# Optimization experiments

Hardware: AMD Instinct MI355X
Metric: run time of the kernel (lower is better)

## Reference

```python
import jax, jax.numpy as jnp
import numpy as np

NUM_CODES = 4096
TEMPERATURE = 1.0
EPS = 1e-08


def setup_inputs() -> dict:
    key = jax.random.key(0)
    k1, k2, k3 = jax.random.split(key, 3)
    B, D, T = 16, 512, 1500
    encoder_stride = 320
    student_features = jax.random.normal(k1, (B, D, T), dtype=jnp.float32)
    codebook = jax.random.normal(k2, (NUM_CODES, D), dtype=jnp.float32)
    lengths = jax.random.randint(k3, (B,), 0, T * encoder_stride, dtype=jnp.int64)
    return {
        "student_features": student_features,
        "codebook": codebook,
        "lengths": lengths,
        "encoder_stride": encoder_stride,
    }


def _length_mask(lengths, T, stride):
    # frame t is valid iff t < floor(length / stride)  -> (B, T) float mask
    n_valid = jnp.minimum(lengths // stride, T)
    return (jnp.arange(T)[None, :] < n_valid[:, None]).astype(jnp.float32)


def reference(student_features, codebook, lengths, encoder_stride):
    B, D, T = student_features.shape
    mask = _length_mask(lengths, T, encoder_stride)            # (B, T)
    z = jnp.transpose(student_features, (0, 2, 1)).reshape(-1, D)  # (N, D), N = B*T
    # Euclidean cdist via ||z||^2 + ||c||^2 - 2 z c^T (same as torch.cdist GEMM path)
    z2 = jnp.sum(z * z, axis=-1, keepdims=True)                # (N, 1)
    c2 = jnp.sum(codebook * codebook, axis=-1)                 # (K,)
    d2 = z2 + c2[None, :] - 2.0 * (z @ codebook.T)             # (N, K)
    distances = jnp.sqrt(jnp.maximum(d2, 1e-12))
    logits = -distances / TEMPERATURE
    probs = jax.nn.softmax(logits, axis=-1)                    # (N, K)
    probs_masked = probs * mask.reshape(-1, 1)
    code_dist = jnp.sum(probs_masked, axis=0)                  # (K,)
    code_dist = code_dist / (jnp.sum(code_dist) + EPS)
    entropy = -jnp.sum(code_dist * jnp.log(code_dist + EPS))
    max_entropy = jnp.log(jnp.float32(NUM_CODES))
    return 1.0 - entropy / max_entropy
```

## Files before the change

kernel.cpp:

```cpp
#include <hip/hip_runtime.h>
#include <hip/hip_bf16.h>

#define NUM_B   16
#define DIM     512
#define TT      1500
#define NROWS   (NUM_B * TT)
#define NCODES  4096
#define ROW_TILES ((NROWS + 127) / 128)
#define NROWS_PAD (ROW_TILES * 128)
#define NSLICE  8
#define SHIFTC  30.0f

typedef __bf16 bf16x8 __attribute__((ext_vector_type(8)));
typedef float  floatx4 __attribute__((ext_vector_type(4)));
typedef unsigned short ushortx8 __attribute__((ext_vector_type(8)));

__device__ __forceinline__ void glds16(const void* g, void* l) {
    __builtin_amdgcn_global_load_lds(
        (__attribute__((address_space(1))) void*)(void*)g,
        (__attribute__((address_space(3))) void*)l, 16, 0, 0);
}

__global__ void k_transpose(const float* __restrict__ sf, unsigned short* __restrict__ zbf,
                            float* __restrict__ z2) {
    __shared__ float tile[32][33];
    int tid = threadIdx.x;
    int b = blockIdx.z, d0 = blockIdx.y * 32, t0 = blockIdx.x * 32;
    int tl = tid & 31, dg = tid >> 5;
#pragma unroll
    for (int p = 0; p < 4; ++p) {
        int dl = p * 8 + dg;
        int t = t0 + tl;
        if (t < TT) tile[tl][dl] = sf[(size_t)(b * DIM + d0 + dl) * TT + t];
    }
    __syncthreads();
    int dl = tid & 31, tg = tid >> 5;
#pragma unroll
    for (int p = 0; p < 4; ++p) {
        int tl2 = p * 8 + tg;
        int t = t0 + tl2;
        float ssq = 0.f;
        if (t < TT) {
            __hip_bfloat16 h = __float2bfloat16(tile[tl2][dl]);
            zbf[(size_t)(b * TT + t) * DIM + d0 + dl] = __builtin_bit_cast(unsigned short, h);
            float vb = __bfloat162float(h);
            ssq = vb * vb;
        }
        ssq += __shfl_xor(ssq, 16); ssq += __shfl_xor(ssq, 8);
        ssq += __shfl_xor(ssq, 4);  ssq += __shfl_xor(ssq, 2);
        ssq += __shfl_xor(ssq, 1);
        if (dl == 0 && t < TT) atomicAdd(&z2[b * TT + t], ssq);
    }
}

__global__ void k_cb(const float* __restrict__ cb, unsigned short* __restrict__ cbbf,
                     float* __restrict__ c2) {
    int k = blockIdx.x * 4 + (threadIdx.x >> 6);
    int lane = threadIdx.x & 63;
    const float4* src = (const float4*)(cb + (size_t)k * DIM + lane * 8);
    float4 a = src[0], b2 = src[1];
    float vals[8] = {a.x, a.y, a.z, a.w, b2.x, b2.y, b2.z, b2.w};
    float s = 0.f;
    unsigned int h[8];
#pragma unroll
    for (int i = 0; i < 8; ++i) {
        __hip_bfloat16 hb = __float2bfloat16(vals[i]);
        h[i] = __builtin_bit_cast(unsigned short, hb);
        float vb = __bfloat162float(hb);
        s += vb * vb;
    }
    uint4 o;
    o.x = h[0] | (h[1] << 16); o.y = h[2] | (h[3] << 16);
    o.z = h[4] | (h[5] << 16); o.w = h[6] | (h[7] << 16);
    *(uint4*)(cbbf + (size_t)k * DIM + lane * 8) = o;
#pragma unroll
    for (int off = 32; off >= 1; off >>= 1) s += __shfl_down(s, off);
    if (lane == 0) c2[k] = s;
}

__global__ __launch_bounds__(256, 2) void k_gemm1(
    const unsigned short* __restrict__ zbf, const unsigned short* __restrict__ cbbf,
    const float* __restrict__ z2, const float* __restrict__ c2,
    const int* __restrict__ lengths, const int* __restrict__ stride_p,
    float* __restrict__ Sg, unsigned short* __restrict__ Eg) {
    __shared__ unsigned short As[128 * 64];
    __shared__ unsigned short Bs[128 * 64];
    __shared__ float z2s[128], c2s[128];
    __shared__ unsigned char vldp[128];
    __shared__ int s_any;
    int tid = threadIdx.x;
    int r0 = blockIdx.y * 128, c0 = blockIdx.x * 128;
    if (tid == 0) s_any = 0;
    __syncthreads();
    if (tid < 128) {
        int n = r0 + tid;
        int valid = 0;
        if (n < NROWS) {
            int b = n / TT, t = n - b * TT;
            int stride = stride_p[0];
            int nv = lengths[b] / stride;
            if (nv > TT) nv = TT;
            valid = (t < nv);
        }
        if (valid) atomicOr(&s_any, 1);
        vldp[tid] = (unsigned char)valid;
        z2s[tid] = z2[r0 + tid];
        c2s[tid] = c2[c0 + tid];
    }
    __syncthreads();
    if (!s_any) return;

    int wave = tid >> 6, lane = tid & 63;
    int l15 = lane & 15, l4 = lane >> 4;
    int wr = (wave >> 1) * 64, wc = (wave & 1) * 64;

    int srow = lane >> 3;
    int scg = (lane & 7) ^ srow;
    const unsigned short* ag = zbf + (size_t)(r0 + wave * 32 + srow) * DIM + scg * 8;
    const unsigned short* bg = cbbf + (size_t)(c0 + wave * 32 + srow) * DIM + scg * 8;
    unsigned short* al = As + (wave * 32) * 64;
    unsigned short* bl = Bs + (wave * 32) * 64;

    floatx4 acc[4][4];
    const floatx4 zero = {0.f, 0.f, 0.f, 0.f};
#pragma unroll
    for (int i = 0; i < 4; ++i)
#pragma unroll
        for (int j = 0; j < 4; ++j) acc[i][j] = zero;

    int sw = l15 & 7;

    for (int kc = 0; kc < 8; ++kc) {
#pragma unroll
        for (int q = 0; q < 4; ++q) {
            glds16(ag + (size_t)q * 8 * DIM + kc * 64, al + q * 8 * 64);
            glds16(bg + (size_t)q * 8 * DIM + kc * 64, bl + q * 8 * 64);
        }
        __syncthreads();
#pragma unroll
        for (int ks = 0; ks < 64; ks += 32) {
            int g = (ks >> 3) + l4;
            int pcg = g ^ sw;
            bf16x8 av[4], bv[4];
#pragma unroll
            for (int i = 0; i < 4; ++i)
                av[i] = __builtin_bit_cast(bf16x8,
                    *(const ushortx8*)&As[(wr + 16 * i + l15) * 64 + pcg * 8]);
#pragma unroll
            for (int j = 0; j < 4; ++j)
                bv[j] = __builtin_bit_cast(bf16x8,
                    *(const ushortx8*)&Bs[(wc + 16 * j + l15) * 64 + pcg * 8]);
#pragma unroll
            for (int i = 0; i < 4; ++i)
#pragma unroll
                for (int j = 0; j < 4; ++j)
                    acc[i][j] = __builtin_amdgcn_mfma_f32_16x16x32_bf16(av[i], bv[j], acc[i][j], 0, 0, 0);
        }
        __syncthreads();
    }

#pragma unroll
    for (int i = 0; i < 4; ++i) {
#pragma unroll
        for (int r = 0; r < 4; ++r) {
            int rl = wr + 16 * i + 4 * l4 + r;
            bool rv = vldp[rl] != 0;
            float z2v = z2s[rl];
            float s = 0.f;
            unsigned int hh[4];
#pragma unroll
            for (int j = 0; j < 4; ++j) {
                int cl = wc + 16 * j + l15;
                float d2 = fmaf(-2.0f, acc[i][j][r], z2v + c2s[cl]);
                float d = sqrtf(fmaxf(d2, 1e-12f));
                float e = __expf(SHIFTC - d);
                s += e;
                hh[j] = __builtin_bit_cast(unsigned short, __float2bfloat16(e));
            }
            if (rv) {
                uint2 pk;
                pk.x = hh[0] | (hh[1] << 16);
                pk.y = hh[2] | (hh[3] << 16);
                *(uint2*)(Eg + (size_t)(r0 + rl) * NCODES + c0 + wc + l15 * 4) = pk;
            }
            s += __shfl_xor(s, 1); s += __shfl_xor(s, 2);
            s += __shfl_xor(s, 4); s += __shfl_xor(s, 8);
            if (l15 == 0 && rv) atomicAdd(&Sg[r0 + rl], s);
        }
    }
}

__global__ __launch_bounds__(256) void k_scan(
    const unsigned short* __restrict__ Eg, const float* __restrict__ Sg,
    const int* __restrict__ lengths, const int* __restrict__ stride_p,
    float* __restrict__ cdp) {
    __shared__ float rs[32];
    __shared__ int s_any;
    int tid = threadIdx.x;
    int r0 = blockIdx.y * 32;
    if (tid == 0) s_any = 0;
    __syncthreads();
    if (tid < 32) {
        int n = r0 + tid;
        int valid = 0;
        if (n < NROWS) {
            int b = n / TT, t = n - b * TT;
            int nv = lengths[b] / stride_p[0];
            if (nv > TT) nv = TT;
            valid = (t < nv);
        }
        if (valid) atomicOr(&s_any, 1);
        rs[tid] = valid ? 1.0f / Sg[n] : 0.0f;
    }
    __syncthreads();
    if (!s_any) return;

    int p0 = blockIdx.x * 2048 + tid * 8;
    float acc[8] = {0.f, 0.f, 0.f, 0.f, 0.f, 0.f, 0.f, 0.f};
    for (int nn = 0; nn < 32; ++nn) {
        float rn = rs[nn];
        if (rn == 0.f) continue;
        uint4 v = *(const uint4*)(Eg + (size_t)(r0 + nn) * NCODES + p0);
        unsigned int u[4] = {v.x, v.y, v.z, v.w};
#pragma unroll
        for (int q = 0; q < 4; ++q) {
            acc[2 * q]     += rn * __builtin_bit_cast(float, u[q] << 16);
            acc[2 * q + 1] += rn * __builtin_bit_cast(float, u[q] & 0xffff0000u);
        }
    }
    int gbase = p0 & ~63;
    int l15a = (p0 & 63) >> 2;
    float* outp = cdp + (size_t)(blockIdx.y & (NSLICE - 1)) * NCODES;
#pragma unroll
    for (int t = 0; t < 8; ++t) {
        int col = gbase + 16 * (t & 3) + l15a + (t >> 2);
        atomicAdd(&outp[col], acc[t]);
    }
}

template <int PASS>
__global__ __launch_bounds__(256, 2) void k_gemm(
    const unsigned short* __restrict__ zbf, const unsigned short* __restrict__ cbbf,
    const float* __restrict__ z2, const float* __restrict__ c2,
    const int* __restrict__ lengths, const int* __restrict__ stride_p,
    float* __restrict__ Sg, float* __restrict__ cd) {
    __shared__ unsigned short As[128 * 64];
    __shared__ unsigned short Bs[128 * 64];
    __shared__ float z2s[128], c2s[128], rs[128];
    __shared__ int s_any;
    int tid = threadIdx.x;
    int r0 = blockIdx.y * 128, c0 = blockIdx.x * 128;
    if (tid == 0) s_any = 0;
    __syncthreads();
    if (tid < 128) {
        int n = r0 + tid;
        int valid = 0;
        if (n < NROWS) {
            int b = n / TT, t = n - b * TT;
            int stride = stride_p[0];
            int nv = lengths[b] / stride;
            if (nv > TT) nv = TT;
            valid = (t < nv);
        }
        if (valid) atomicOr(&s_any, 1);
        z2s[tid] = z2[r0 + tid];
        c2s[tid] = c2[c0 + tid];
        if (PASS == 2) rs[tid] = valid ? (1.0f / Sg[r0 + tid]) : 0.0f;
    }
    __syncthreads();
    if (!s_any) return;

    int wave = tid >> 6, lane = tid & 63;
    int l15 = lane & 15, l4 = lane >> 4;
    int wr = (wave >> 1) * 64, wc = (wave & 1) * 64;
    int srow = lane >> 3;
    int scg = (lane & 7) ^ srow;
    const unsigned short* ag = zbf + (size_t)(r0 + wave * 32 + srow) * DIM + scg * 8;
    const unsigned short* bg = cbbf + (size_t)(c0 + wave * 32 + srow) * DIM + scg * 8;
    unsigned short* al = As + (wave * 32) * 64;
    unsigned short* bl = Bs + (wave * 32) * 64;

    floatx4 acc[4][4];
    const floatx4 zero = {0.f, 0.f, 0.f, 0.f};
#pragma unroll
    for (int i = 0; i < 4; ++i)
#pragma unroll
        for (int j = 0; j < 4; ++j) acc[i][j] = zero;
    int sw = l15 & 7;
    for (int kc = 0; kc < 8; ++kc) {
#pragma unroll
        for (int q = 0; q < 4; ++q) {
            glds16(ag + (size_t)q * 8 * DIM + kc * 64, al + q * 8 * 64);
            glds16(bg + (size_t)q * 8 * DIM + kc * 64, bl + q * 8 * 64);
        }
        __syncthreads();
#pragma unroll
        for (int ks = 0; ks < 64; ks += 32) {
            int g = (ks >> 3) + l4;
            int pcg = g ^ sw;
            bf16x8 av[4], bv[4];
#pragma unroll
            for (int i = 0; i < 4; ++i)
                av[i] = __builtin_bit_cast(bf16x8, *(const ushortx8*)&As[(wr + 16 * i + l15) * 64 + pcg * 8]);
#pragma unroll
            for (int j = 0; j < 4; ++j)
                bv[j] = __builtin_bit_cast(bf16x8, *(const ushortx8*)&Bs[(wc + 16 * j + l15) * 64 + pcg * 8]);
#pragma unroll
            for (int i = 0; i < 4; ++i)
#pragma unroll
                for (int j = 0; j < 4; ++j)
                    acc[i][j] = __builtin_amdgcn_mfma_f32_16x16x32_bf16(av[i], bv[j], acc[i][j], 0, 0, 0);
        }
        __syncthreads();
    }
    if (PASS == 1) {
#pragma unroll
        for (int i = 0; i < 4; ++i) {
#pragma unroll
            for (int r = 0; r < 4; ++r) {
                int rl = wr + 16 * i + 4 * l4 + r;
                float z2v = z2s[rl];
                float s = 0.f;
#pragma unroll
                for (int j = 0; j < 4; ++j) {
                    int cl = wc + 16 * j + l15;
                    float d2 = z2v + c2s[cl] - 2.0f * acc[i][j][r];
                    float d = sqrtf(fmaxf(d2, 1e-12f));
                    s += __expf(SHIFTC - d);
                }
                s += __shfl_xor(s, 1); s += __shfl_xor(s, 2);
                s += __shfl_xor(s, 4); s += __shfl_xor(s, 8);
                if (l15 == 0) atomicAdd(&Sg[r0 + rl], s);
            }
        }
    } else {
#pragma unroll
        for (int j = 0; j < 4; ++j) {
            int cl = wc + 16 * j + l15;
            float c2v = c2s[cl];
            float cs = 0.f;
#pragma unroll
            for (int i = 0; i < 4; ++i) {
#pragma unroll
                for (int r = 0; r < 4; ++r) {
                    int rl = wr + 16 * i + 4 * l4 + r;
                    float d2 = z2s[rl] + c2v - 2.0f * acc[i][j][r];
                    float d = sqrtf(fmaxf(d2, 1e-12f));
                    cs += __expf(SHIFTC - d) * rs[rl];
                }
            }
            cs += __shfl_xor(cs, 16); cs += __shfl_xor(cs, 32);
            if (l4 == 0) atomicAdd(&cd[c0 + cl], cs);
        }
    }
}

__global__ __launch_bounds__(1024) void k_final(const float* __restrict__ cdp,
                                                float* __restrict__ out) {
    __shared__ float red[16];
    __shared__ float tot_s;
    int tid = threadIdx.x, lane = tid & 63, wave = tid >> 6;
    float vloc[4];
    float t = 0.f;
#pragma unroll
    for (int q = 0; q < 4; ++q) {
        int i = tid + q * 1024;
        float v = 0.f;
#pragma unroll
        for (int s = 0; s < NSLICE; ++s) v += cdp[(size_t)s * NCODES + i];
        vloc[q] = v;
        t += v;
    }
#pragma unroll
    for (int off = 32; off >= 1; off >>= 1) t += __shfl_down(t, off);
    if (lane == 0) red[wave] = t;
    __syncthreads();
    if (tid == 0) {
        float tt = 0.f;
#pragma unroll
        for (int w = 0; w < 16; ++w) tt += red[w];
        tot_s = tt;
    }
    __syncthreads();
    float inv = 1.0f / (tot_s + 1e-8f);
    float e = 0.f;
#pragma unroll
    for (int q = 0; q < 4; ++q) {
        float p = vloc[q] * inv;
        e += p * __logf(p + 1e-8f);
    }
#pragma unroll
    for (int off = 32; off >= 1; off >>= 1) e += __shfl_down(e, off);
    if (lane == 0) red[wave] = e;
    __syncthreads();
    if (tid == 0) {
        float ee = 0.f;
#pragma unroll
        for (int w = 0; w < 16; ++w) ee += red[w];
        out[0] = 1.0f - (-ee) / __logf((float)NCODES);
    }
}

extern "C" void kernel_launch(void* const* d_in, const int* in_sizes, int n_in,
                              void* d_out, int out_size, void* d_ws, size_t ws_size,
                              hipStream_t stream) {
    const float* sf = (const float*)d_in[0];
    const float* cb = (const float*)d_in[1];
    const int* lengths = (const int*)d_in[2];
    const int* stride_p = (const int*)d_in[3];

    float* Sg = (float*)d_ws;
    float* cdp = Sg + NROWS_PAD;
    float* z2 = cdp + (size_t)NSLICE * NCODES;
    float* c2 = z2 + NROWS_PAD;
    unsigned short* zbf = (unsigned short*)(c2 + NCODES);
    unsigned short* cbbf = zbf + (size_t)NROWS_PAD * DIM;
    unsigned short* Eg = cbbf + (size_t)NCODES * DIM;

    size_t base_bytes = (size_t)(2 * NROWS_PAD + NCODES) * 4
                      + (size_t)NSLICE * NCODES * 4
                      + ((size_t)NROWS_PAD * DIM + (size_t)NCODES * DIM) * 2;
    size_t need = base_bytes + (size_t)NROWS_PAD * NCODES * 2;

    hipMemsetAsync(Sg, 0, ((size_t)2 * NROWS_PAD + (size_t)NSLICE * NCODES) * sizeof(float), stream);
    k_transpose<<<dim3((TT + 31) / 32, DIM / 32, NUM_B), 256, 0, stream>>>(sf, zbf, z2);
    k_cb<<<dim3(NCODES / 4), 256, 0, stream>>>(cb, cbbf, c2);
    if (ws_size >= need) {
        k_gemm1<<<dim3(NCODES / 128, ROW_TILES), 256, 0, stream>>>(zbf, cbbf, z2, c2, lengths, stride_p, Sg, Eg);
        k_scan<<<dim3(NCODES / 2048, NROWS_PAD / 32), 256, 0, stream>>>(Eg, Sg, lengths, stride_p, cdp);
    } else {
        k_gemm<1><<<dim3(NCODES / 128, ROW_TILES), 256, 0, stream>>>(zbf, cbbf, z2, c2, lengths, stride_p, Sg, cdp);
        k_gemm<2><<<dim3(NCODES / 128, ROW_TILES), 256, 0, stream>>>(zbf, cbbf, z2, c2, lengths, stride_p, Sg, cdp);
    }
    k_final<<<1, 1024, 0, stream>>>(cdp, (float*)d_out);
}
```

Baseline: 236.2 us.

## Widen transpose stores, store E columns in natural order, widen scan per block

The transpose kernel now handles 64 feature dims per block, and each thread converts 8 values and writes them as one 16-byte vector, replacing scattered 2-byte stores. The GEMM epilogue now writes each exp value to its true column with 2-byte stores instead of a packed 8-byte store in permuted order. The scan kernel then reads contiguous 16 columns per thread and covers all 4096 codes in one block per 32-row group, dropping the column remapping. The aim is better-coalesced transpose writes and simpler scan indexing, but the GEMM now issues narrower scattered stores for the large E buffer, and the scan issues more atomics per thread.

```diff
diff --git a/kernel.cpp b/kernel.cpp
--- a/kernel.cpp
+++ b/kernel.cpp
@@ -21,36 +21,39 @@
         (__attribute__((address_space(3))) void*)l, 16, 0, 0);
 }
 
-__global__ void k_transpose(const float* __restrict__ sf, unsigned short* __restrict__ zbf,
-                            float* __restrict__ z2) {
-    __shared__ float tile[32][33];
+__global__ __launch_bounds__(256) void k_transpose(
+    const float* __restrict__ sf, unsigned short* __restrict__ zbf,
+    float* __restrict__ z2) {
+    __shared__ float tile[32][68];
     int tid = threadIdx.x;
-    int b = blockIdx.z, d0 = blockIdx.y * 32, t0 = blockIdx.x * 32;
+    int b = blockIdx.z, d0 = blockIdx.y * 64, t0 = blockIdx.x * 32;
     int tl = tid & 31, dg = tid >> 5;
 #pragma unroll
-    for (int p = 0; p < 4; ++p) {
-        int dl = p * 8 + dg;
+    for (int dd = 0; dd < 8; ++dd) {
+        int d = dd * 8 + dg;
         int t = t0 + tl;
-        if (t < TT) tile[tl][dl] = sf[(size_t)(b * DIM + d0 + dl) * TT + t];
-    }
-    __syncthreads();
-    int dl = tid & 31, tg = tid >> 5;
-#pragma unroll
-    for (int p = 0; p < 4; ++p) {
-        int tl2 = p * 8 + tg;
-        int t = t0 + tl2;
-        float ssq = 0.f;
-        if (t < TT) {
-            __hip_bfloat16 h = __float2bfloat16(tile[tl2][dl]);
-            zbf[(size_t)(b * TT + t) * DIM + d0 + dl] = __builtin_bit_cast(unsigned short, h);
-            float vb = __bfloat162float(h);
-            ssq = vb * vb;
-        }
-        ssq += __shfl_xor(ssq, 16); ssq += __shfl_xor(ssq, 8);
-        ssq += __shfl_xor(ssq, 4);  ssq += __shfl_xor(ssq, 2);
-        ssq += __shfl_xor(ssq, 1);
-        if (dl == 0 && t < TT) atomicAdd(&z2[b * TT + t], ssq);
-    }
+        if (t < TT) tile[tl][d] = sf[(size_t)(b * DIM + d0 + d) * TT + t];
+    }
+    __syncthreads();
+    int t = tid >> 3, dgrp = tid & 7;
+    int tglob = t0 + t;
+    float ssq = 0.f;
+    if (tglob < TT) {
+        unsigned int h[8];
+#pragma unroll
+        for (int i = 0; i < 8; ++i) {
+            __hip_bfloat16 hb = __float2bfloat16(tile[t][dgrp * 8 + i]);
+            h[i] = __builtin_bit_cast(unsigned short, hb);
+            float vb = __bfloat162float(hb);
+            ssq += vb * vb;
+        }
+        uint4 o;
+        o.x = h[0] | (h[1] << 16); o.y = h[2] | (h[3] << 16);
+        o.z = h[4] | (h[5] << 16); o.w = h[6] | (h[7] << 16);
+        *(uint4*)(zbf + (size_t)(b * TT + tglob) * DIM + d0 + dgrp * 8) = o;
+    }
+    ssq += __shfl_xor(ssq, 1); ssq += __shfl_xor(ssq, 2); ssq += __shfl_xor(ssq, 4);
+    if (dgrp == 0 && tglob < TT) atomicAdd(&z2[b * TT + tglob], ssq);
 }
 
 __global__ void k_cb(const float* __restrict__ cb, unsigned short* __restrict__ cbbf,
@@ -167,21 +170,15 @@
             bool rv = vldp[rl] != 0;
             float z2v = z2s[rl];
             float s = 0.f;
-            unsigned int hh[4];
+            unsigned short* Ep = Eg + (size_t)(r0 + rl) * NCODES + c0 + wc + l15;
 #pragma unroll
             for (int j = 0; j < 4; ++j) {
                 int cl = wc + 16 * j + l15;
-                float d2 = fmaf(-2.0f, acc[i][j][r], z2v + c2s[cl]);
+                float d2 = z2v + c2s[cl] - 2.0f * acc[i][j][r];
                 float d = sqrtf(fmaxf(d2, 1e-12f));
                 float e = __expf(SHIFTC - d);
                 s += e;
-                hh[j] = __builtin_bit_cast(unsigned short, __float2bfloat16(e));
-            }
-            if (rv) {
-                uint2 pk;
-                pk.x = hh[0] | (hh[1] << 16);
-                pk.y = hh[2] | (hh[3] << 16);
-                *(uint2*)(Eg + (size_t)(r0 + rl) * NCODES + c0 + wc + l15 * 4) = pk;
+                if (rv) Ep[16 * j] = __builtin_bit_cast(unsigned short, __float2bfloat16(e));
             }
             s += __shfl_xor(s, 1); s += __shfl_xor(s, 2);
             s += __shfl_xor(s, 4); s += __shfl_xor(s, 8);
@@ -197,7 +194,7 @@
     __shared__ float rs[32];
     __shared__ int s_any;
     int tid = threadIdx.x;
-    int r0 = blockIdx.y * 32;
+    int r0 = blockIdx.x * 32;
     if (tid == 0) s_any = 0;
     __syncthreads();
     if (tid < 32) {
@@ -215,27 +212,25 @@
     __syncthreads();
     if (!s_any) return;
 
-    int p0 = blockIdx.x * 2048 + tid * 8;
-    float acc[8] = {0.f, 0.f, 0.f, 0.f, 0.f, 0.f, 0.f, 0.f};
+    int col0 = tid * 16;
+    float acc[16];
+#pragma unroll
+    for (int t = 0; t < 16; ++t) acc[t] = 0.f;
     for (int nn = 0; nn < 32; ++nn) {
         float rn = rs[nn];
         if (rn == 0.f) continue;
-        uint4 v = *(const uint4*)(Eg + (size_t)(r0 + nn) * NCODES + p0);
-        unsigned int u[4] = {v.x, v.y, v.z, v.w};
-#pragma unroll
-        for (int q = 0; q < 4; ++q) {
+        const uint4* p = (const uint4*)(Eg + (size_t)(r0 + nn) * NCODES + col0);
+        uint4 v0 = p[0], v1 = p[1];
+        unsigned int u[8] = {v0.x, v0.y, v0.z, v0.w, v1.x, v1.y, v1.z, v1.w};
+#pragma unroll
+        for (int q = 0; q < 8; ++q) {
             acc[2 * q]     += rn * __builtin_bit_cast(float, u[q] << 16);
             acc[2 * q + 1] += rn * __builtin_bit_cast(float, u[q] & 0xffff0000u);
         }
     }
-    int gbase = p0 & ~63;
-    int l15a = (p0 & 63) >> 2;
-    float* outp = cdp + (size_t)(blockIdx.y & (NSLICE - 1)) * NCODES;
-#pragma unroll
-    for (int t = 0; t < 8; ++t) {
-        int col = gbase + 16 * (t & 3) + l15a + (t >> 2);
-        atomicAdd(&outp[col], acc[t]);
-    }
+    float* outp = cdp + (size_t)(blockIdx.x & (NSLICE - 1)) * NCODES;
+#pragma unroll
+    for (int t = 0; t < 16; ++t) atomicAdd(&outp[col0 + t], acc[t]);
 }
 
 template <int PASS>
@@ -423,11 +418,11 @@
     size_t need = base_bytes + (size_t)NROWS_PAD * NCODES * 2;
 
     hipMemsetAsync(Sg, 0, ((size_t)2 * NROWS_PAD + (size_t)NSLICE * NCODES) * sizeof(float), stream);
-    k_transpose<<<dim3((TT + 31) / 32, DIM / 32, NUM_B), 256, 0, stream>>>(sf, zbf, z2);
+    k_transpose<<<dim3((TT + 31) / 32, DIM / 64, NUM_B), 256, 0, stream>>>(sf, zbf, z2);
     k_cb<<<dim3(NCODES / 4), 256, 0, stream>>>(cb, cbbf, c2);
     if (ws_size >= need) {
         k_gemm1<<<dim3(NCODES / 128, ROW_TILES), 256, 0, stream>>>(zbf, cbbf, z2, c2, lengths, stride_p, Sg, Eg);
-        k_scan<<<dim3(NCODES / 2048, NROWS_PAD / 32), 256, 0, stream>>>(Eg, Sg, lengths, stride_p, cdp);
+        k_scan<<<dim3(NROWS_PAD / 32), 256, 0, stream>>>(Eg, Sg, lengths, stride_p, cdp);
     } else {
         k_gemm<1><<<dim3(NCODES / 128, ROW_TILES), 256, 0, stream>>>(zbf, cbbf, z2, c2, lengths, stride_p, Sg, cdp);
         k_gemm<2><<<dim3(NCODES / 128, ROW_TILES), 256, 0, stream>>>(zbf, cbbf, z2, c2, lengths, stride_p, Sg, cdp);
```

After: 276.2 us. 1.17x slower.
